# Performance work log

Hardware: AMD Instinct MI355X
Metric: run time of the kernel (lower is better)

Reference implementation:

```python
import jax, jax.numpy as jnp
import numpy as np

# dims: L layers, D d_model, H heads, DH head_dim, DFF ffn, V vocab, BLK nf4 blocksize
L, D, H, DH, DFF, V, BLK = 2, 2048, 16, 128, 5504, 32000, 64
B, S, C, T = 4, 1000, 7, 45

# bitsandbytes NF4 codebook (fixed 16 quantiles of N(0,1), normalized to [-1,1])
NF4 = jnp.array([-1.0, -0.6961928009986877, -0.5250730514526367, -0.39491748809814453,
                 -0.28444138169288635, -0.18477343022823334, -0.09105003625154495, 0.0,
                 0.07958029955625534, 0.16093020141124725, 0.24611230194568634,
                 0.3379152417182922, 0.44070982933044434, 0.5626170039176941,
                 0.7229568362236023, 1.0], dtype=jnp.float32)


def _dequant(idx, scale):
    # idx: [out, in] int in [0,16); scale: [out, in//BLK] per-block absmax
    o, i = idx.shape
    return (NF4[idx].reshape(o, i // BLK, BLK) * scale[:, :, None]).reshape(o, i)


def _rmsnorm(h, w, eps=1e-5):
    return h * jax.lax.rsqrt(jnp.mean(h * h, axis=-1, keepdims=True) + eps) * w


def _rot_half(x):
    x1, x2 = jnp.split(x, 2, axis=-1)
    return jnp.concatenate([-x2, x1], axis=-1)


def _llama_fwd(token_ids, embed, wq_idx, wq_scale, wk_idx, wk_scale, wv_idx, wv_scale,
               wo_idx, wo_scale, wg_idx, wg_scale, wu_idx, wu_scale, wd_idx, wd_scale,
               ln1_w, ln2_w, lnf_w):
    Bt, St = token_ids.shape
    h = embed[token_ids]  # [B,S,D]
    # rotary embeddings
    inv = 1.0 / (10000.0 ** (jnp.arange(0, DH, 2, dtype=jnp.float32) / DH))
    ang = jnp.arange(St, dtype=jnp.float32)[:, None] * inv[None, :]  # [S, DH/2]
    emb_ang = jnp.concatenate([ang, ang], axis=-1)  # [S, DH]
    cos, sin = jnp.cos(emb_ang), jnp.sin(emb_ang)
    mask = jnp.where(jnp.tril(jnp.ones((St, St), dtype=bool)), 0.0, -1e9)  # causal
    for l in range(L):
        xn = _rmsnorm(h, ln1_w[l])
        q = (xn @ _dequant(wq_idx[l], wq_scale[l]).T).reshape(Bt, St, H, DH).transpose(0, 2, 1, 3)
        k = (xn @ _dequant(wk_idx[l], wk_scale[l]).T).reshape(Bt, St, H, DH).transpose(0, 2, 1, 3)
        v = (xn @ _dequant(wv_idx[l], wv_scale[l]).T).reshape(Bt, St, H, DH).transpose(0, 2, 1, 3)
        q = q * cos + _rot_half(q) * sin
        k = k * cos + _rot_half(k) * sin
        att = jax.nn.softmax(jnp.einsum('bhqd,bhkd->bhqk', q, k) / np.float32(np.sqrt(DH)) + mask, axis=-1)
        ctx = jnp.einsum('bhqk,bhkd->bhqd', att, v).transpose(0, 2, 1, 3).reshape(Bt, St, D)
        h = h + ctx @ _dequant(wo_idx[l], wo_scale[l]).T
        xn = _rmsnorm(h, ln2_w[l])
        g = xn @ _dequant(wg_idx[l], wg_scale[l]).T
        u = xn @ _dequant(wu_idx[l], wu_scale[l]).T
        h = h + (jax.nn.silu(g) * u) @ _dequant(wd_idx[l], wd_scale[l]).T
    # hidden_states[-1].mean(dim=1)
    return _rmsnorm(h, lnf_w).mean(axis=1)


def setup_inputs() -> dict:
    key = jax.random.key(0)
    ks = jax.random.split(key, 20)
    ridx = lambda k, shp: jax.random.randint(k, shp, 0, 16, dtype=jnp.int32)
    rsc = lambda k, shp: jax.random.uniform(k, shp, minval=0.01, maxval=0.03, dtype=jnp.float32)
    return {
        'x': jax.random.normal(ks[0], (B, C, T), dtype=jnp.float32),
        'token_ids': jax.random.randint(ks[1], (B, S), 0, V, dtype=jnp.int32),
        'embed': jax.random.normal(ks[2], (V, D), dtype=jnp.float32) * 0.02,
        'wq_idx': ridx(ks[3], (L, D, D)), 'wq_scale': rsc(ks[4], (L, D, D // BLK)),
        'wk_idx': ridx(ks[5], (L, D, D)), 'wk_scale': rsc(ks[6], (L, D, D // BLK)),
        'wv_idx': ridx(ks[7], (L, D, D)), 'wv_scale': rsc(ks[8], (L, D, D // BLK)),
        'wo_idx': ridx(ks[9], (L, D, D)), 'wo_scale': rsc(ks[10], (L, D, D // BLK)),
        'wg_idx': ridx(ks[11], (L, DFF, D)), 'wg_scale': rsc(ks[12], (L, DFF, D // BLK)),
        'wu_idx': ridx(ks[13], (L, DFF, D)), 'wu_scale': rsc(ks[14], (L, DFF, D // BLK)),
        'wd_idx': ridx(ks[15], (L, D, DFF)), 'wd_scale': rsc(ks[16], (L, D, DFF // BLK)),
        'ln1_w': jnp.ones((L, D), dtype=jnp.float32),
        'ln2_w': jnp.ones((L, D), dtype=jnp.float32),
        'lnf_w': jnp.ones((D,), dtype=jnp.float32),
        'proj_w': jax.random.normal(ks[17], (D, T), dtype=jnp.float32) * 0.05,
        'proj_b': jnp.zeros((D,), dtype=jnp.float32),
    }


def reference(x, token_ids, embed, wq_idx, wq_scale, wk_idx, wk_scale, wv_idx, wv_scale,
              wo_idx, wo_scale, wg_idx, wg_scale, wu_idx, wu_scale, wd_idx, wd_scale,
              ln1_w, ln2_w, lnf_w, proj_w, proj_b):
    # NF4-quantized Llama-style causal LM forward + mean pool over sequence
    e_text = _llama_fwd(token_ids, embed, wq_idx, wq_scale, wk_idx, wk_scale, wv_idx, wv_scale,
                        wo_idx, wo_scale, wg_idx, wg_scale, wu_idx, wu_scale, wd_idx, wd_scale,
                        ln1_w, ln2_w, lnf_w)  # [B, D]
    # series branch: channel-mean -> linear -> L2 normalize
    series_mean = x.mean(axis=1)  # [B, T]
    series_emb = series_mean @ proj_w.T + proj_b  # [B, D]
    series_emb = series_emb / jnp.maximum(jnp.linalg.norm(series_emb, axis=-1, keepdims=True), 1e-12)
    return e_text + series_emb
```

## Files before the change

kernel.cpp:

```cpp
#include <hip/hip_runtime.h>
#include <hip/hip_bf16.h>

#define L_N 2
#define D_ 2048
#define H_ 16
#define DH_ 128
#define DFF_ 5504
#define B_ 4
#define S_ 1000
#define C_ 7
#define T_ 45
#define M_ 4000

typedef short bf16x8 __attribute__((ext_vector_type(8)));
typedef float f32x4 __attribute__((ext_vector_type(4)));

__constant__ float NF4_TAB[16] = {
  -1.0f, -0.6961928009986877f, -0.5250730514526367f, -0.39491748809814453f,
  -0.28444138169288635f, -0.18477343022823334f, -0.09105003625154495f, 0.0f,
  0.07958029955625534f, 0.16093020141124725f, 0.24611230194568634f,
  0.3379152417182922f, 0.44070982933044434f, 0.5626170039176941f,
  0.7229568362236023f, 1.0f };

__device__ __forceinline__ unsigned short f2bf(float f) {
  unsigned int u = __float_as_uint(f);
  u += 0x7fffu + ((u >> 16) & 1u);
  return (unsigned short)(u >> 16);
}
__device__ __forceinline__ float bf2f(unsigned short u) {
  return __uint_as_float(((unsigned int)u) << 16);
}
__device__ __forceinline__ f32x4 zero4() { f32x4 z; z[0]=0.f; z[1]=0.f; z[2]=0.f; z[3]=0.f; return z; }
__device__ __forceinline__ f32x4 mfma16(bf16x8 a, bf16x8 b, f32x4 c) {
  return __builtin_amdgcn_mfma_f32_16x16x32_bf16(a, b, c, 0, 0, 0);
}

typedef __attribute__((address_space(3))) unsigned int lds_u32;
typedef const __attribute__((address_space(1))) unsigned int glb_u32;
__device__ __forceinline__ void gload16(const void* g, void* l) {
  __builtin_amdgcn_global_load_lds((glb_u32*)g, (lds_u32*)l, 16, 0, 0);
}

__global__ void rope_tables(float* __restrict__ cosT, float* __restrict__ sinT) {
  int s = blockIdx.x, d = threadIdx.x;
  int j = d & 63;
  float inv = expf(-(float)j * (9.210340371976184f / 64.f));
  float ang = (float)s * inv;
  cosT[s * DH_ + d] = cosf(ang);
  sinT[s * DH_ + d] = sinf(ang);
}

__global__ __launch_bounds__(256) void embed_gather(const int* __restrict__ tok,
    const float* __restrict__ emb, float* __restrict__ h) {
  int row = blockIdx.x;
  int tk = tok[row];
  const float4* src = reinterpret_cast<const float4*>(emb + (size_t)tk * D_);
  float4* dst = reinterpret_cast<float4*>(h + (size_t)row * D_);
  dst[threadIdx.x] = src[threadIdx.x];
  dst[threadIdx.x + 256] = src[threadIdx.x + 256];
}

__global__ __launch_bounds__(256) void rmsnorm_k(const float* __restrict__ h,
    const float* __restrict__ w, unsigned short* __restrict__ out) {
  const int row = blockIdx.x, t = threadIdx.x;
  const float* hp = h + (size_t)row * D_;
  float4 a = *reinterpret_cast<const float4*>(&hp[t * 8]);
  float4 b = *reinterpret_cast<const float4*>(&hp[t * 8 + 4]);
  float ss = a.x*a.x + a.y*a.y + a.z*a.z + a.w*a.w
           + b.x*b.x + b.y*b.y + b.z*b.z + b.w*b.w;
#pragma unroll
  for (int m = 1; m < 64; m <<= 1) ss += __shfl_xor(ss, m);
  __shared__ float red[4];
  if ((t & 63) == 0) red[t >> 6] = ss;
  __syncthreads();
  float tot = red[0] + red[1] + red[2] + red[3];
  float rs = rsqrtf(tot * (1.0f / D_) + 1e-5f);
  float4 wa = *reinterpret_cast<const float4*>(&w[t * 8]);
  float4 wb = *reinterpret_cast<const float4*>(&w[t * 8 + 4]);
  unsigned r0 = (unsigned)f2bf(a.x*rs*wa.x) | ((unsigned)f2bf(a.y*rs*wa.y) << 16);
  unsigned r1 = (unsigned)f2bf(a.z*rs*wa.z) | ((unsigned)f2bf(a.w*rs*wa.w) << 16);
  unsigned r2 = (unsigned)f2bf(b.x*rs*wb.x) | ((unsigned)f2bf(b.y*rs*wb.y) << 16);
  unsigned r3 = (unsigned)f2bf(b.z*rs*wb.z) | ((unsigned)f2bf(b.w*rs*wb.w) << 16);
  int4 ov; ov.x = (int)r0; ov.y = (int)r1; ov.z = (int)r2; ov.w = (int)r3;
  *reinterpret_cast<int4*>(&out[(size_t)row * D_ + t * 8]) = ov;
}

struct DqJob { const int* idx; const float* sc; unsigned short* out; };
struct DqBatch { DqJob j[4]; };

__global__ __launch_bounds__(256) void dequant_batch(DqBatch bt, int K) {
  __shared__ float nf4[16];
  const int t = threadIdx.x;
  if (t < 16) nf4[t] = NF4_TAB[t];
  __syncthreads();
  const DqJob jb = bt.j[blockIdx.z];
  const int row = blockIdx.y;
  const int k0 = blockIdx.x * 2048 + t * 8;
  if (k0 >= K) return;
  const size_t base = (size_t)row * K + k0;
  int4 a = *reinterpret_cast<const int4*>(&jb.idx[base]);
  int4 b = *reinterpret_cast<const int4*>(&jb.idx[base + 4]);
  float s = jb.sc[(size_t)row * (K >> 6) + (k0 >> 6)];
  unsigned r0 = (unsigned)f2bf(nf4[a.x & 15] * s) | ((unsigned)f2bf(nf4[a.y & 15] * s) << 16);
  unsigned r1 = (unsigned)f2bf(nf4[a.z & 15] * s) | ((unsigned)f2bf(nf4[a.w & 15] * s) << 16);
  unsigned r2 = (unsigned)f2bf(nf4[b.x & 15] * s) | ((unsigned)f2bf(nf4[b.y & 15] * s) << 16);
  unsigned r3 = (unsigned)f2bf(nf4[b.z & 15] * s) | ((unsigned)f2bf(nf4[b.w & 15] * s) << 16);
  int4 ov; ov.x = (int)r0; ov.y = (int)r1; ov.z = (int)r2; ov.w = (int)r3;
  *reinterpret_cast<int4*>(&jb.out[base]) = ov;
}

template<int MODE, int GROUPED>
__global__ __launch_bounds__(256, 4) void gemm_bf16(
    const unsigned short* __restrict__ A,
    const unsigned short* __restrict__ Bw,
    int Mdim, int N, int K, int nx,
    void* outp, const unsigned short* gin) {
  __shared__ unsigned short A_lds[128 * 64];
  __shared__ unsigned short B_lds[128 * 64];
  const int t = threadIdx.x;
  const int lane = t & 63, wid = t >> 6;

  int m_blk, n_blk;
  const int bid = blockIdx.x;
  if (GROUPED) {
    const int xcd = bid & 7, l = bid >> 3;
    m_blk = xcd * 4 + (l & 3);
    n_blk = l >> 2;
  } else {
    const int nwg = gridDim.x;
    const int wg = (bid & 7) * (nwg >> 3) + (bid >> 3);
    n_blk = wg % nx;
    m_blk = wg / nx;
  }
  const int n0 = n_blk * 128;
  const int m0 = m_blk * 128;

  const int wm = (wid >> 1) * 64, wn = (wid & 1) * 64;
  const int lr = lane & 15, lg = lane >> 4;
  const int lrow = lane >> 3;
  const int lslot = (((lane & 7) ^ lrow) << 4);
  const int rswz = (lr & 7) << 4;

  f32x4 acc[4][4];
#pragma unroll
  for (int i = 0; i < 4; ++i)
#pragma unroll
    for (int j = 0; j < 4; ++j) acc[i][j] = zero4();

  const int kT = K >> 6;
  const size_t rowb = (size_t)(K * 2);

  for (int kt = 0; kt < kT; ++kt) {
#pragma unroll
    for (int c0 = 0; c0 < 4; ++c0) {
      const int c = wid + 4 * c0;
      int gr = m0 + c * 8 + lrow;
      gr = gr < Mdim ? gr : Mdim - 1;
      gload16((const char*)A + (size_t)gr * rowb + kt * 128 + lslot,
              (char*)&A_lds[0] + c * 1024);
      const int nr = n0 + c * 8 + lrow;
      gload16((const char*)Bw + (size_t)nr * rowb + kt * 128 + lslot,
              (char*)&B_lds[0] + c * 1024);
    }
    __syncthreads();
#pragma unroll
    for (int ks = 0; ks < 2; ++ks) {
      bf16x8 af[4], bfr[4];
      const int cb = (ks * 64 + lg * 16) ^ rswz;
#pragma unroll
      for (int i = 0; i < 4; ++i) {
        af[i]  = *reinterpret_cast<const bf16x8*>(
                   (const char*)&A_lds[0] + (wm + i * 16 + lr) * 128 + cb);
        bfr[i] = *reinterpret_cast<const bf16x8*>(
                   (const char*)&B_lds[0] + (wn + i * 16 + lr) * 128 + cb);
      }
      __builtin_amdgcn_s_setprio(1);
#pragma unroll
      for (int mi = 0; mi < 4; ++mi)
#pragma unroll
        for (int ni = 0; ni < 4; ++ni)
          acc[mi][ni] = mfma16(af[mi], bfr[ni], acc[mi][ni]);
      __builtin_amdgcn_s_setprio(0);
    }
    __syncthreads();
  }

#pragma unroll
  for (int mi = 0; mi < 4; ++mi) {
#pragma unroll
    for (int r = 0; r < 4; ++r) {
      int gm = m0 + wm + mi * 16 + lg * 4 + r;
      if (gm >= Mdim) continue;
#pragma unroll
      for (int ni = 0; ni < 4; ++ni) {
        int gn = n0 + wn + ni * 16 + lr;
        float v = acc[mi][ni][r];
        if (MODE == 0) {
          ((unsigned short*)outp)[(size_t)gm * N + gn] = f2bf(v);
        } else if (MODE == 1) {
          const int which = gn >> 11;
          const int hh = (gn >> 7) & 15, dd = gn & 127;
          const int b = gm / S_, s = gm - b * S_;
          ((unsigned short*)outp)[
            (((size_t)which * (B_ * H_) + b * H_ + hh) * S_ + s) * DH_ + dd] = f2bf(v);
        } else if (MODE == 2) {
          float g = bf2f(gin[(size_t)gm * N + gn]);
          float sg = g / (1.f + __expf(-g));
          ((unsigned short*)outp)[(size_t)gm * N + gn] = f2bf(sg * v);
        } else {
          ((float*)outp)[(size_t)gm * N + gn] += v;
        }
      }
    }
  }
}

__global__ __launch_bounds__(256) void rope_apply(unsigned short* __restrict__ qb,
    unsigned short* __restrict__ kb, const float* __restrict__ cosT,
    const float* __restrict__ sinT) {
  size_t i = (size_t)blockIdx.x * 256 + threadIdx.x;
  int d = (int)(i & 63);
  size_t row = i >> 6;
  int s = (int)(row % S_);
  size_t base = row * DH_;
  float c = cosT[s * DH_ + d], sn = sinT[s * DH_ + d];
  float q0 = bf2f(qb[base + d]), q1 = bf2f(qb[base + d + 64]);
  qb[base + d]      = f2bf(q0 * c - q1 * sn);
  qb[base + d + 64] = f2bf(q1 * c + q0 * sn);
  float k0 = bf2f(kb[base + d]), k1 = bf2f(kb[base + d + 64]);
  kb[base + d]      = f2bf(k0 * c - k1 * sn);
  kb[base + d + 64] = f2bf(k1 * c + k0 * sn);
}

__global__ __launch_bounds__(256) void vtrans_k(const unsigned short* __restrict__ vb,
    unsigned short* __restrict__ vt) {
  __shared__ unsigned int tile[64][33];
  const int t = threadIdx.x;
  const int s0 = blockIdx.x * 64, d0 = blockIdx.y * 64, bh = blockIdx.z;
#pragma unroll
  for (int j = 0; j < 2; ++j) {
    int idx = t + 256 * j;
    int s_r = idx >> 3, c8 = (idx & 7) << 3;
    int srow = s0 + s_r; srow = srow < S_ ? srow : S_ - 1;
    int4 v = *reinterpret_cast<const int4*>(&vb[((size_t)bh * S_ + srow) * DH_ + d0 + c8]);
    tile[s_r][(c8 >> 1) + 0] = (unsigned)v.x;
    tile[s_r][(c8 >> 1) + 1] = (unsigned)v.y;
    tile[s_r][(c8 >> 1) + 2] = (unsigned)v.z;
    tile[s_r][(c8 >> 1) + 3] = (unsigned)v.w;
  }
  __syncthreads();
#pragma unroll
  for (int j = 0; j < 2; ++j) {
    int idx = t + 256 * j;
    int d_r = idx >> 3, s8 = (idx & 7) << 3;
    unsigned r[8];
#pragma unroll
    for (int e = 0; e < 8; ++e) {
      unsigned wv = tile[s8 + e][d_r >> 1];
      r[e] = (d_r & 1) ? (wv >> 16) : (wv & 0xffffu);
    }
    int4 ov;
    ov.x = (int)(r[0] | (r[1] << 16));
    ov.y = (int)(r[2] | (r[3] << 16));
    ov.z = (int)(r[4] | (r[5] << 16));
    ov.w = (int)(r[6] | (r[7] << 16));
    *reinterpret_cast<int4*>(&vt[((size_t)(bh * 128 + d0 + d_r)) * 1024 + s0 + s8]) = ov;
  }
}

__global__ __launch_bounds__(512, 4) void attn2_k(const unsigned short* __restrict__ qg,
    const unsigned short* __restrict__ kg, const unsigned short* __restrict__ vtg,
    unsigned short* __restrict__ ctx) {
  __shared__ unsigned short K_lds[64 * 128];
  __shared__ unsigned short VT_lds[128 * 64];
  const int t = threadIdx.x, lane = t & 63, w = t >> 6;
  const int lr = lane & 15, lg = lane >> 4;
  const int bh = blockIdx.x, qt = blockIdx.y;
  const int q0 = qt * 128;
  const int b = bh >> 4, hh = bh & 15;
  const size_t kbase2 = (size_t)bh * S_ * DH_ * 2;
  const int q_idx = q0 + w * 16 + lr;
  const int swz = (lr & 7) << 4;

  bf16x8 qf[4];
#pragma unroll
  for (int ks = 0; ks < 4; ++ks) {
    bf16x8 z;
#pragma unroll
    for (int e = 0; e < 8; ++e) z[e] = 0;
    if (q_idx < S_)
      z = *reinterpret_cast<const bf16x8*>(
            (const char*)qg + kbase2 + (size_t)q_idx * 256 + ks * 64 + lg * 16);
    qf[ks] = z;
  }
  float mst = -1e30f, lst = 0.f;
  f32x4 cacc[8];
#pragma unroll
  for (int f = 0; f < 8; ++f) cacc[f] = zero4();

  const int q_hi = (q0 + 127 < S_) ? q0 + 127 : S_ - 1;
  const int nt = q_hi / 64 + 1;
  const int wq_max = q0 + w * 16 + 15;

  for (int kt = 0; kt < nt; ++kt) {
    const int kv0 = kt * 64;
    __syncthreads();
#pragma unroll
    for (int j = 0; j < 2; ++j) {
      const int chunk = w + 8 * j;
      int krow = chunk * 4 + (lane >> 4);
      int kcolb = (lane & 15) << 4;
      int gr = kv0 + krow; gr = gr < S_ ? gr : S_ - 1;
      gload16((const char*)kg + kbase2 + (size_t)gr * 256 + (kcolb ^ ((krow & 7) << 4)),
              (char*)K_lds + chunk * 1024);
      int vrow = chunk * 8 + (lane >> 3);
      int vcolb = (lane & 7) << 4;
      gload16((const char*)vtg + ((size_t)(bh * 128 + vrow) * 1024 + kv0) * 2 + (vcolb ^ ((vrow & 7) << 4)),
              (char*)VT_lds + chunk * 1024);
    }
    __syncthreads();
    if (kv0 > wq_max) continue;

    f32x4 sacc[4];
#pragma unroll
    for (int c = 0; c < 4; ++c) sacc[c] = zero4();
#pragma unroll
    for (int ks = 0; ks < 4; ++ks) {
#pragma unroll
      for (int c = 0; c < 4; ++c) {
        bf16x8 kf = *reinterpret_cast<const bf16x8*>(
            &K_lds[(c * 16 + lr) * 128 + (((ks * 64 + lg * 16) ^ swz) >> 1)]);
        sacc[c] = mfma16(kf, qf[ks], sacc[c]);
      }
    }
    float p[4][4];
    float mx = -1e30f;
#pragma unroll
    for (int c = 0; c < 4; ++c)
#pragma unroll
      for (int r = 0; r < 4; ++r) {
        int kv = kv0 + c * 16 + lg * 4 + r;
        float v = sacc[c][r] * 0.08838834764831845f;
        if (kv > q_idx || kv >= S_) v = -1e30f;
        p[c][r] = v;
        mx = fmaxf(mx, v);
      }
    mx = fmaxf(mx, __shfl_xor(mx, 16));
    mx = fmaxf(mx, __shfl_xor(mx, 32));
    float mn = fmaxf(mst, mx);
    float corr = __expf(mst - mn);
    mst = mn;
    float rs = 0.f;
#pragma unroll
    for (int c = 0; c < 4; ++c)
#pragma unroll
      for (int r = 0; r < 4; ++r) {
        float e = __expf(p[c][r] - mn);
        p[c][r] = e;
        rs += e;
      }
    rs += __shfl_xor(rs, 16);
    rs += __shfl_xor(rs, 32);
    lst = lst * corr + rs;
#pragma unroll
    for (int f = 0; f < 8; ++f)
#pragma unroll
      for (int r = 0; r < 4; ++r) cacc[f][r] *= corr;

    unsigned pk01[4], pk23[4];
#pragma unroll
    for (int c = 0; c < 4; ++c) {
      pk01[c] = (unsigned)f2bf(p[c][0]) | ((unsigned)f2bf(p[c][1]) << 16);
      pk23[c] = (unsigned)f2bf(p[c][2]) | ((unsigned)f2bf(p[c][3]) << 16);
    }
#pragma unroll
    for (int ks = 0; ks < 2; ++ks) {
      unsigned bu[4];
#pragma unroll
      for (int jj = 0; jj < 4; ++jj) {
        const int srcl = ((lg & 1) * 2 + (jj >> 1)) * 16 + lr;
        unsigned lo = (unsigned)__shfl((int)((jj & 1) ? pk23[2 * ks]     : pk01[2 * ks]),     srcl);
        unsigned hi = (unsigned)__shfl((int)((jj & 1) ? pk23[2 * ks + 1] : pk01[2 * ks + 1]), srcl);
        bu[jj] = (lg >= 2) ? hi : lo;
      }
      union { unsigned u[4]; bf16x8 v; } pb;
      pb.u[0] = bu[0]; pb.u[1] = bu[1]; pb.u[2] = bu[2]; pb.u[3] = bu[3];
#pragma unroll
      for (int f = 0; f < 8; ++f) {
        bf16x8 vtf = *reinterpret_cast<const bf16x8*>(
            &VT_lds[(f * 16 + lr) * 64 + (((ks * 64 + lg * 16) ^ swz) >> 1)]);
        cacc[f] = mfma16(vtf, pb.v, cacc[f]);
      }
    }
  }

  if (q_idx < S_) {
    float inv = 1.f / lst;
    unsigned short* cp = ctx + ((size_t)(b * S_ + q_idx)) * D_ + hh * 128;
#pragma unroll
    for (int f = 0; f < 8; ++f) {
      unsigned lo = (unsigned)f2bf(cacc[f][0] * inv) | ((unsigned)f2bf(cacc[f][1] * inv) << 16);
      unsigned hi = (unsigned)f2bf(cacc[f][2] * inv) | ((unsigned)f2bf(cacc[f][3] * inv) << 16);
      uint2 ov; ov.x = lo; ov.y = hi;
      *reinterpret_cast<uint2*>(cp + f * 16 + lg * 4) = ov;
    }
  }
}

__global__ __launch_bounds__(256) void meanpool(const unsigned short* __restrict__ xn,
    float* __restrict__ out) {
  int d = blockIdx.x * 256 + threadIdx.x;
  int b = blockIdx.y;
  const unsigned short* p = xn + (size_t)b * S_ * D_ + d;
  float s = 0.f;
  for (int i = 0; i < S_; ++i) s += bf2f(p[(size_t)i * D_]);
  out[(size_t)b * D_ + d] = s * (1.f / S_);
}

__global__ __launch_bounds__(256) void series_k(const float* __restrict__ x,
    const float* __restrict__ pw, const float* __restrict__ pb, float* out) {
  __shared__ float sm[T_];
  __shared__ float emb[D_];
  __shared__ float red[4];
  int b = blockIdx.x, t = threadIdx.x;
  if (t < T_) {
    float s = 0.f;
    for (int c = 0; c < C_; ++c) s += x[((size_t)b * C_ + c) * T_ + t];
    sm[t] = s * (1.f / C_);
  }
  __syncthreads();
  float ssq = 0.f;
#pragma unroll
  for (int j = 0; j < D_ / 256; ++j) {
    int d = j * 256 + t;
    float e = pb[d];
    for (int tt = 0; tt < T_; ++tt) e += sm[tt] * pw[(size_t)d * T_ + tt];
    emb[d] = e;
    ssq += e * e;
  }
#pragma unroll
  for (int m = 1; m < 64; m <<= 1) ssq += __shfl_xor(ssq, m);
  if ((t & 63) == 0) red[t >> 6] = ssq;
  __syncthreads();
  float tot = red[0] + red[1] + red[2] + red[3];
  float inv = 1.f / fmaxf(sqrtf(tot), 1e-12f);
#pragma unroll
  for (int j = 0; j < D_ / 256; ++j) {
    int d = j * 256 + t;
    out[(size_t)b * D_ + d] += emb[d] * inv;
  }
}

extern "C" void kernel_launch(void* const* d_in, const int* in_sizes, int n_in,
                              void* d_out, int out_size, void* d_ws, size_t ws_size,
                              hipStream_t stream) {
  const float* x      = (const float*)d_in[0];
  const int*   tok    = (const int*)d_in[1];
  const float* embedw = (const float*)d_in[2];
  const int*   wq_idx = (const int*)d_in[3];
  const float* wq_sc  = (const float*)d_in[4];
  const int*   wk_idx = (const int*)d_in[5];
  const float* wk_sc  = (const float*)d_in[6];
  const int*   wv_idx = (const int*)d_in[7];
  const float* wv_sc  = (const float*)d_in[8];
  const int*   wo_idx = (const int*)d_in[9];
  const float* wo_sc  = (const float*)d_in[10];
  const int*   wg_idx = (const int*)d_in[11];
  const float* wg_sc  = (const float*)d_in[12];
  const int*   wu_idx = (const int*)d_in[13];
  const float* wu_sc  = (const float*)d_in[14];
  const int*   wd_idx = (const int*)d_in[15];
  const float* wd_sc  = (const float*)d_in[16];
  const float* ln1    = (const float*)d_in[17];
  const float* ln2    = (const float*)d_in[18];
  const float* lnf    = (const float*)d_in[19];
  const float* projw  = (const float*)d_in[20];
  const float* projb  = (const float*)d_in[21];
  float* out = (float*)d_out;
  (void)in_sizes; (void)n_in; (void)out_size; (void)ws_size;

  char* wsp = (char*)d_ws;
  size_t off = 0;
  auto alloc = [&](size_t bytes) -> void* {
    void* p = wsp + off; off += (bytes + 255) & ~(size_t)255; return p; };
  float* cosT = (float*)alloc((size_t)S_ * DH_ * 4);
  float* sinT = (float*)alloc((size_t)S_ * DH_ * 4);
  float* hbuf = (float*)alloc((size_t)M_ * D_ * 4);
  unsigned short* xn   = (unsigned short*)alloc((size_t)M_ * D_ * 2);
  unsigned short* qkv  = (unsigned short*)alloc((size_t)3 * B_ * H_ * S_ * DH_ * 2);
  unsigned short* wdeq = (unsigned short*)alloc((size_t)2 * DFF_ * D_ * 2);
  unsigned short* vt   = (unsigned short*)alloc((size_t)B_ * H_ * DH_ * 1024 * 2);
  const size_t NH = (size_t)B_ * H_ * S_ * DH_;
  unsigned short* qb = qkv, *kb = qkv + NH, *vb = qkv + 2 * NH;
  unsigned short* ctx  = xn;
  unsigned short* gbuf = qkv;

  rope_tables<<<S_, DH_, 0, stream>>>(cosT, sinT);
  embed_gather<<<M_, 256, 0, stream>>>(tok, embedw, hbuf);

  const int my = (M_ + 127) / 128;
  const dim3 gQKV((3 * D_ / 128) * my);
  const dim3 gAtt((D_ / 128) * my);
  const dim3 gMlp((DFF_ / 128) * my);
  const size_t DD = (size_t)D_ * D_;
  const size_t FD = (size_t)DFF_ * D_;

  for (int l = 0; l < L_N; ++l) {
    const int*   wqi = wq_idx + (size_t)l * DD;
    const float* wqs = wq_sc + (size_t)l * D_ * (D_ / 64);
    const int*   wki = wk_idx + (size_t)l * DD;
    const float* wks = wk_sc + (size_t)l * D_ * (D_ / 64);
    const int*   wvi = wv_idx + (size_t)l * DD;
    const float* wvs = wv_sc + (size_t)l * D_ * (D_ / 64);
    const int*   woi = wo_idx + (size_t)l * DD;
    const float* wos = wo_sc + (size_t)l * D_ * (D_ / 64);
    const int*   wgi = wg_idx + (size_t)l * FD;
    const float* wgs = wg_sc + (size_t)l * DFF_ * (D_ / 64);
    const int*   wui = wu_idx + (size_t)l * FD;
    const float* wus = wu_sc + (size_t)l * DFF_ * (D_ / 64);
    const int*   wdi = wd_idx + (size_t)l * FD;
    const float* wds = wd_sc + (size_t)l * D_ * (DFF_ / 64);

    rmsnorm_k<<<M_, 256, 0, stream>>>(hbuf, ln1 + l * D_, xn);

    {
      DqBatch bt;
      bt.j[0] = { wqi, wqs, wdeq };
      bt.j[1] = { wki, wks, wdeq + DD };
      bt.j[2] = { wvi, wvs, wdeq + 2 * DD };
      bt.j[3] = { woi, wos, wdeq + 3 * DD };
      dequant_batch<<<dim3(1, D_, 4), 256, 0, stream>>>(bt, D_);
    }
    gemm_bf16<1, 1><<<gQKV, 256, 0, stream>>>(xn, wdeq, M_, 3 * D_, D_, 3 * D_ / 128,
                                              qkv, nullptr);
    rope_apply<<<(B_ * H_ * S_ * 64) / 256, 256, 0, stream>>>(qb, kb, cosT, sinT);
    vtrans_k<<<dim3(16, 2, B_ * H_), 256, 0, stream>>>(vb, vt);
    attn2_k<<<dim3(B_ * H_, 8), 512, 0, stream>>>(qb, kb, vt, ctx);
    gemm_bf16<3, 1><<<gAtt, 256, 0, stream>>>(ctx, wdeq + 3 * DD, M_, D_, D_, D_ / 128,
                                              hbuf, nullptr);
    rmsnorm_k<<<M_, 256, 0, stream>>>(hbuf, ln2 + l * D_, xn);

    {
      DqBatch bt;
      bt.j[0] = { wgi, wgs, wdeq };
      bt.j[1] = { wui, wus, wdeq + FD };
      bt.j[2] = bt.j[0]; bt.j[3] = bt.j[0];
      dequant_batch<<<dim3(1, DFF_, 2), 256, 0, stream>>>(bt, D_);
    }
    gemm_bf16<0, 1><<<gMlp, 256, 0, stream>>>(xn, wdeq, M_, DFF_, D_, DFF_ / 128,
                                              gbuf, nullptr);
    gemm_bf16<2, 0><<<gMlp, 256, 0, stream>>>(xn, wdeq + FD, M_, DFF_, D_, DFF_ / 128,
                                              gbuf, gbuf);

    {
      DqBatch bt;
      bt.j[0] = { wdi, wds, wdeq };
      bt.j[1] = bt.j[0]; bt.j[2] = bt.j[0]; bt.j[3] = bt.j[0];
      dequant_batch<<<dim3(3, D_, 1), 256, 0, stream>>>(bt, DFF_);
    }
    gemm_bf16<3, 1><<<gAtt, 256, 0, stream>>>(gbuf, wdeq, M_, D_, DFF_, D_ / 128,
                                              hbuf, nullptr);
  }

  rmsnorm_k<<<M_, 256, 0, stream>>>(hbuf, lnf, xn);
  meanpool<<<dim3(D_ / 256, B_), 256, 0, stream>>>(xn, out);
  series_k<<<B_, 256, 0, stream>>>(x, projw, projb, out);
}
```

Measured before the change: 1.340 ms.

## Split-K residual GEMMs, merge gate/up launches, fuse partial-sum add into rmsnorm

The output-projection and down-projection GEMMs now split K across two z-slices. One slice accumulates into the residual and the other writes a float scratch buffer, which the following rmsnorm adds back into the residual. Gate and up projections run in a single launch using blockIdx.z to choose the weights, followed by a separate SiLU-multiply kernel. The goal is to double parallelism for the small-N residual GEMMs (only 512 tiles) and overlap the two MLP GEMMs. The cost is extra scratch traffic and an extra elementwise pass over the M×DFF activations.

```diff
diff --git a/kernel.cpp b/kernel.cpp
--- a/kernel.cpp
+++ b/kernel.cpp
@@ -60,12 +60,22 @@
   dst[threadIdx.x + 256] = src[threadIdx.x + 256];
 }
 
-__global__ __launch_bounds__(256) void rmsnorm_k(const float* __restrict__ h,
-    const float* __restrict__ w, unsigned short* __restrict__ out) {
+__global__ __launch_bounds__(256) void rmsnorm_k(float* __restrict__ h,
+    const float* __restrict__ add, const float* __restrict__ w,
+    unsigned short* __restrict__ out) {
   const int row = blockIdx.x, t = threadIdx.x;
-  const float* hp = h + (size_t)row * D_;
+  float* hp = h + (size_t)row * D_;
   float4 a = *reinterpret_cast<const float4*>(&hp[t * 8]);
   float4 b = *reinterpret_cast<const float4*>(&hp[t * 8 + 4]);
+  if (add) {
+    const float* ap = add + (size_t)row * D_;
+    float4 da = *reinterpret_cast<const float4*>(&ap[t * 8]);
+    float4 db = *reinterpret_cast<const float4*>(&ap[t * 8 + 4]);
+    a.x += da.x; a.y += da.y; a.z += da.z; a.w += da.w;
+    b.x += db.x; b.y += db.y; b.z += db.z; b.w += db.w;
+    *reinterpret_cast<float4*>(&hp[t * 8]) = a;
+    *reinterpret_cast<float4*>(&hp[t * 8 + 4]) = b;
+  }
   float ss = a.x*a.x + a.y*a.y + a.z*a.z + a.w*a.w
            + b.x*b.x + b.y*b.y + b.z*b.z + b.w*b.w;
 #pragma unroll
@@ -109,29 +119,26 @@
   *reinterpret_cast<int4*>(&jb.out[base]) = ov;
 }
 
-template<int MODE, int GROUPED>
+template<int MODE>
 __global__ __launch_bounds__(256, 4) void gemm_bf16(
     const unsigned short* __restrict__ A,
     const unsigned short* __restrict__ Bw,
-    int Mdim, int N, int K, int nx,
-    void* outp, const unsigned short* gin) {
+    const unsigned short* __restrict__ Bw2,
+    int Mdim, int N, int K, int nx, int ksplit,
+    void* outp, void* outp2, float* dscr) {
   __shared__ unsigned short A_lds[128 * 64];
   __shared__ unsigned short B_lds[128 * 64];
   const int t = threadIdx.x;
   const int lane = t & 63, wid = t >> 6;
-
-  int m_blk, n_blk;
+  const int z = blockIdx.z;
+
+  const unsigned short* Bsrc = (MODE == 0 && z) ? Bw2 : Bw;
+  void* osel = (MODE == 0 && z) ? outp2 : outp;
+
   const int bid = blockIdx.x;
-  if (GROUPED) {
-    const int xcd = bid & 7, l = bid >> 3;
-    m_blk = xcd * 4 + (l & 3);
-    n_blk = l >> 2;
-  } else {
-    const int nwg = gridDim.x;
-    const int wg = (bid & 7) * (nwg >> 3) + (bid >> 3);
-    n_blk = wg % nx;
-    m_blk = wg / nx;
-  }
+  const int xcd = bid & 7, l = bid >> 3;
+  const int m_blk = xcd * 4 + (l & 3);
+  const int n_blk = l >> 2;
   const int n0 = n_blk * 128;
   const int m0 = m_blk * 128;
 
@@ -148,9 +155,11 @@
     for (int j = 0; j < 4; ++j) acc[i][j] = zero4();
 
   const int kT = K >> 6;
+  const int ktlo = (MODE == 3) ? (z ? ksplit : 0) : 0;
+  const int kthi = (MODE == 3) ? (z ? kT : ksplit) : kT;
   const size_t rowb = (size_t)(K * 2);
 
-  for (int kt = 0; kt < kT; ++kt) {
+  for (int kt = ktlo; kt < kthi; ++kt) {
 #pragma unroll
     for (int c0 = 0; c0 < 4; ++c0) {
       const int c = wid + 4 * c0;
@@ -159,7 +168,7 @@
       gload16((const char*)A + (size_t)gr * rowb + kt * 128 + lslot,
               (char*)&A_lds[0] + c * 1024);
       const int nr = n0 + c * 8 + lrow;
-      gload16((const char*)Bw + (size_t)nr * rowb + kt * 128 + lslot,
+      gload16((const char*)Bsrc + (size_t)nr * rowb + kt * 128 + lslot,
               (char*)&B_lds[0] + c * 1024);
     }
     __syncthreads();
@@ -196,23 +205,40 @@
         int gn = n0 + wn + ni * 16 + lr;
         float v = acc[mi][ni][r];
         if (MODE == 0) {
-          ((unsigned short*)outp)[(size_t)gm * N + gn] = f2bf(v);
+          ((unsigned short*)osel)[(size_t)gm * N + gn] = f2bf(v);
         } else if (MODE == 1) {
           const int which = gn >> 11;
           const int hh = (gn >> 7) & 15, dd = gn & 127;
           const int b = gm / S_, s = gm - b * S_;
           ((unsigned short*)outp)[
             (((size_t)which * (B_ * H_) + b * H_ + hh) * S_ + s) * DH_ + dd] = f2bf(v);
-        } else if (MODE == 2) {
-          float g = bf2f(gin[(size_t)gm * N + gn]);
-          float sg = g / (1.f + __expf(-g));
-          ((unsigned short*)outp)[(size_t)gm * N + gn] = f2bf(sg * v);
         } else {
-          ((float*)outp)[(size_t)gm * N + gn] += v;
+          if (z == 0) ((float*)outp)[(size_t)gm * N + gn] += v;
+          else        dscr[(size_t)gm * N + gn] = v;
         }
       }
     }
   }
+}
+
+__global__ __launch_bounds__(256) void silu_mul(unsigned short* __restrict__ g,
+    const unsigned short* __restrict__ u) {
+  const size_t i = ((size_t)blockIdx.x * 256 + threadIdx.x) * 8;
+  int4 gv = *reinterpret_cast<const int4*>(&g[i]);
+  int4 uv = *reinterpret_cast<const int4*>(&u[i]);
+  const unsigned* gp = reinterpret_cast<const unsigned*>(&gv);
+  const unsigned* up = reinterpret_cast<const unsigned*>(&uv);
+  unsigned ov[4];
+#pragma unroll
+  for (int j = 0; j < 4; ++j) {
+    float g0 = bf2f(gp[j] & 0xffffu), g1 = bf2f(gp[j] >> 16);
+    float u0 = bf2f(up[j] & 0xffffu), u1 = bf2f(up[j] >> 16);
+    float s0 = g0 / (1.f + __expf(-g0)) * u0;
+    float s1 = g1 / (1.f + __expf(-g1)) * u1;
+    ov[j] = (unsigned)f2bf(s0) | ((unsigned)f2bf(s1) << 16);
+  }
+  int4 o; o.x = (int)ov[0]; o.y = (int)ov[1]; o.z = (int)ov[2]; o.w = (int)ov[3];
+  *reinterpret_cast<int4*>(&g[i]) = o;
 }
 
 __global__ __launch_bounds__(256) void rope_apply(unsigned short* __restrict__ qb,
@@ -490,6 +516,9 @@
   unsigned short* qkv  = (unsigned short*)alloc((size_t)3 * B_ * H_ * S_ * DH_ * 2);
   unsigned short* wdeq = (unsigned short*)alloc((size_t)2 * DFF_ * D_ * 2);
   unsigned short* vt   = (unsigned short*)alloc((size_t)B_ * H_ * DH_ * 1024 * 2);
+  void* R = alloc((size_t)M_ * DFF_ * 2);
+  float* dscr = (float*)R;
+  unsigned short* ubuf = (unsigned short*)R;
   const size_t NH = (size_t)B_ * H_ * S_ * DH_;
   unsigned short* qb = qkv, *kb = qkv + NH, *vb = qkv + 2 * NH;
   unsigned short* ctx  = xn;
@@ -500,8 +529,8 @@
 
   const int my = (M_ + 127) / 128;
   const dim3 gQKV((3 * D_ / 128) * my);
-  const dim3 gAtt((D_ / 128) * my);
-  const dim3 gMlp((DFF_ / 128) * my);
+  const dim3 gAtt((D_ / 128) * my, 1, 2);
+  const dim3 gMlp((DFF_ / 128) * my, 1, 2);
   const size_t DD = (size_t)D_ * D_;
   const size_t FD = (size_t)DFF_ * D_;
 
@@ -521,7 +550,7 @@
     const int*   wdi = wd_idx + (size_t)l * FD;
     const float* wds = wd_sc + (size_t)l * D_ * (DFF_ / 64);
 
-    rmsnorm_k<<<M_, 256, 0, stream>>>(hbuf, ln1 + l * D_, xn);
+    rmsnorm_k<<<M_, 256, 0, stream>>>(hbuf, l == 0 ? nullptr : dscr, ln1 + l * D_, xn);
 
     {
       DqBatch bt;
@@ -531,14 +560,14 @@
       bt.j[3] = { woi, wos, wdeq + 3 * DD };
       dequant_batch<<<dim3(1, D_, 4), 256, 0, stream>>>(bt, D_);
     }
-    gemm_bf16<1, 1><<<gQKV, 256, 0, stream>>>(xn, wdeq, M_, 3 * D_, D_, 3 * D_ / 128,
-                                              qkv, nullptr);
+    gemm_bf16<1><<<gQKV, 256, 0, stream>>>(xn, wdeq, nullptr, M_, 3 * D_, D_,
+                                           3 * D_ / 128, 0, qkv, nullptr, nullptr);
     rope_apply<<<(B_ * H_ * S_ * 64) / 256, 256, 0, stream>>>(qb, kb, cosT, sinT);
     vtrans_k<<<dim3(16, 2, B_ * H_), 256, 0, stream>>>(vb, vt);
     attn2_k<<<dim3(B_ * H_, 8), 512, 0, stream>>>(qb, kb, vt, ctx);
-    gemm_bf16<3, 1><<<gAtt, 256, 0, stream>>>(ctx, wdeq + 3 * DD, M_, D_, D_, D_ / 128,
-                                              hbuf, nullptr);
-    rmsnorm_k<<<M_, 256, 0, stream>>>(hbuf, ln2 + l * D_, xn);
+    gemm_bf16<3><<<gAtt, 256, 0, stream>>>(ctx, wdeq + 3 * DD, nullptr, M_, D_, D_,
+                                           D_ / 128, 16, hbuf, nullptr, dscr);
+    rmsnorm_k<<<M_, 256, 0, stream>>>(hbuf, dscr, ln2 + l * D_, xn);
 
     {
       DqBatch bt;
@@ -547,10 +576,9 @@
       bt.j[2] = bt.j[0]; bt.j[3] = bt.j[0];
       dequant_batch<<<dim3(1, DFF_, 2), 256, 0, stream>>>(bt, D_);
     }
-    gemm_bf16<0, 1><<<gMlp, 256, 0, stream>>>(xn, wdeq, M_, DFF_, D_, DFF_ / 128,
-                                              gbuf, nullptr);
-    gemm_bf16<2, 0><<<gMlp, 256, 0, stream>>>(xn, wdeq + FD, M_, DFF_, D_, DFF_ / 128,
-                                              gbuf, gbuf);
+    gemm_bf16<0><<<gMlp, 256, 0, stream>>>(xn, wdeq, wdeq + FD, M_, DFF_, D_,
+                                           DFF_ / 128, 0, gbuf, ubuf, nullptr);
+    silu_mul<<<(M_ * DFF_ / 8) / 256, 256, 0, stream>>>(gbuf, ubuf);
 
     {
       DqBatch bt;
@@ -558,11 +586,11 @@
       bt.j[1] = bt.j[0]; bt.j[2] = bt.j[0]; bt.j[3] = bt.j[0];
       dequant_batch<<<dim3(3, D_, 1), 256, 0, stream>>>(bt, DFF_);
     }
-    gemm_bf16<3, 1><<<gAtt, 256, 0, stream>>>(gbuf, wdeq, M_, D_, DFF_, D_ / 128,
-                                              hbuf, nullptr);
-  }
-
-  rmsnorm_k<<<M_, 256, 0, stream>>>(hbuf, lnf, xn);
+    gemm_bf16<3><<<gAtt, 256, 0, stream>>>(gbuf, wdeq, nullptr, M_, D_, DFF_,
+                                           D_ / 128, 43, hbuf, nullptr, dscr);
+  }
+
+  rmsnorm_k<<<M_, 256, 0, stream>>>(hbuf, dscr, lnf, xn);
   meanpool<<<dim3(D_ / 256, B_), 256, 0, stream>>>(xn, out);
   series_k<<<B_, 256, 0, stream>>>(x, projw, projb, out);
 }
```

Result: faster. 1.308 ms (-2.4%).
